# Kernel tuning notes

Measured on AMD Instinct MI355X. Metric: run time of the kernel, lower is better.

Reference implementation:

```python
import jax, jax.numpy as jnp
import numpy as np

N_NODES = 100000
N_EDGES = 1600000
F_IN, HIDDEN, N_CLS = 128, 128, 40


def _gcn_layer(h, W, b, src, dst, norm, n):
    # h: [n, d_in] -> linear transform then edge-normalized scatter-add
    h = h @ W                                   # [n, d_out]
    msg = h[src] * norm[:, None]                # gather over edges [E', d_out]
    out = jax.ops.segment_sum(msg, dst, num_segments=n)
    return out + b


def setup_inputs() -> dict:
    key = jax.random.key(0)
    k1, k2, k3, k4 = jax.random.split(key, 4)
    x = jax.random.normal(k1, (N_NODES, F_IN), dtype=jnp.float32)
    edge_index = jax.random.randint(k2, (2, N_EDGES), 0, N_NODES, dtype=jnp.int32)
    # glorot-style init
    W1 = jax.random.normal(k3, (F_IN, HIDDEN), dtype=jnp.float32) * (1.0 / np.sqrt(F_IN))
    W2 = jax.random.normal(k4, (HIDDEN, N_CLS), dtype=jnp.float32) * (1.0 / np.sqrt(HIDDEN))
    b1 = jnp.zeros((HIDDEN,), dtype=jnp.float32)
    b2 = jnp.zeros((N_CLS,), dtype=jnp.float32)
    return {"x": x, "edge_index": edge_index, "W1": W1, "b1": b1,
            "W2": W2, "b2": b2, "dropout": 0}


def reference(x, edge_index, W1, b1, W2, b2, dropout):
    n = x.shape[0]
    src, dst = edge_index[0], edge_index[1]
    # add self loops (PyG GCNConv default)
    loop = jnp.arange(n, dtype=src.dtype)
    src = jnp.concatenate([src, loop])
    dst = jnp.concatenate([dst, loop])
    # symmetric normalization D^{-1/2} (A+I) D^{-1/2}
    deg = jax.ops.segment_sum(jnp.ones(src.shape, dtype=x.dtype), dst, num_segments=n)
    dinv = jnp.where(deg > 0, jax.lax.rsqrt(deg), 0.0)
    norm = dinv[src] * dinv[dst]                # [E + n]
    h = jax.nn.relu(_gcn_layer(x, W1, b1, src, dst, norm, n))
    # F.dropout with training=False is identity (eval mode)
    return _gcn_layer(h, W2, b2, src, dst, norm, n)
```

## Files before the change

kernel.cpp:

```cpp
#include <hip/hip_runtime.h>
#include <stdint.h>


#define NF 128
#define NC 40
#define PSHIFT 7
#define PNODES 128
#define GH 256

typedef __attribute__((ext_vector_type(8))) short short8;
typedef __attribute__((ext_vector_type(4))) float float4m;

__device__ __forceinline__ float bflo2f(unsigned int u) {
  union { unsigned int i; float f; } v; v.i = u << 16; return v.f;
}
__device__ __forceinline__ float bfhi2f(unsigned int u) {
  union { unsigned int i; float f; } v; v.i = u & 0xffff0000u; return v.f;
}
__device__ __forceinline__ unsigned short f2bf(float f) {
  union { float f; unsigned int i; } v; v.f = f;
  unsigned int x = v.i;
  return (unsigned short)((x + 0x7fffu + ((x >> 16) & 1u)) >> 16);
}

__global__ __launch_bounds__(256) void hist_pack_k(
    const int* __restrict__ ei, int* __restrict__ histT, int E, int CPB, int NPART,
    const float* __restrict__ W1, const float* __restrict__ W2,
    unsigned short* __restrict__ Bpack, unsigned short* __restrict__ W2pack) {
  int tid = threadIdx.x, bid = blockIdx.x;
  if (bid >= GH) {
    int g = (bid - GH) * 256 + tid;
    const float* W; unsigned short* dst; int cols, frag;
    if (g < 2048)      { W = W1; dst = Bpack;  cols = 128; frag = g; }
    else if (g < 2816) { W = W2; dst = W2pack; cols = 40;  frag = g - 2048; }
    else return;
    int ct = frag >> 8, ks = (frag >> 6) & 3, lane = frag & 63;
    int quad = lane >> 4, l15 = lane & 15;
    int col = ct * 16 + l15, krow = ks * 32 + quad * 8;
    ushort4 lo = {0,0,0,0}, hi = {0,0,0,0};
    if (col < cols) {
      lo.x = f2bf(W[(krow + 0) * cols + col]);
      lo.y = f2bf(W[(krow + 1) * cols + col]);
      lo.z = f2bf(W[(krow + 2) * cols + col]);
      lo.w = f2bf(W[(krow + 3) * cols + col]);
      hi.x = f2bf(W[(krow + 4) * cols + col]);
      hi.y = f2bf(W[(krow + 5) * cols + col]);
      hi.z = f2bf(W[(krow + 6) * cols + col]);
      hi.w = f2bf(W[(krow + 7) * cols + col]);
    }
    *(ushort4*)&dst[(size_t)frag * 8 + 0] = lo;
    *(ushort4*)&dst[(size_t)frag * 8 + 4] = hi;
    return;
  }
  __shared__ int h[1024];
  for (int i = tid; i < NPART; i += 256) h[i] = 0;
  __syncthreads();
  int e0 = bid * CPB, e1 = min(e0 + CPB, E);
  for (int e = e0 + tid; e < e1; e += 256)
    atomicAdd(&h[ei[E + e] >> PSHIFT], 1);
  __syncthreads();
  for (int i = tid; i < NPART; i += 256) histT[(size_t)i * GH + bid] = h[i];
}

__global__ __launch_bounds__(256) void scanA_k(int* __restrict__ histT,
                                               int* __restrict__ partTotal) {
  __shared__ int sm[GH];
  int tid = threadIdx.x, p = blockIdx.x;
  int v = histT[(size_t)p * GH + tid];
  sm[tid] = v; __syncthreads();
  for (int off = 1; off < GH; off <<= 1) {
    int t = (tid >= off) ? sm[tid - off] : 0;
    __syncthreads();
    sm[tid] += t;
    __syncthreads();
  }
  histT[(size_t)p * GH + tid] = sm[tid] - v;
  if (tid == GH - 1) partTotal[p] = sm[GH - 1];
}

__global__ __launch_bounds__(1024) void scanB_k(const int* __restrict__ partTotal,
                                                int* __restrict__ base, int NPART) {
  __shared__ int sm[1024];
  int tid = threadIdx.x;
  int v = (tid < NPART) ? partTotal[tid] : 0;
  sm[tid] = v; __syncthreads();
  for (int off = 1; off < 1024; off <<= 1) {
    int t = (tid >= off) ? sm[tid - off] : 0;
    __syncthreads();
    sm[tid] += t;
    __syncthreads();
  }
  if (tid < NPART) base[tid] = sm[tid] - v;
}

__global__ __launch_bounds__(256) void scatter_k(const int* __restrict__ ei,
                                                 const int* __restrict__ histT,
                                                 const int* __restrict__ base,
                                                 unsigned int* __restrict__ epart,
                                                 int E, int CPB, int NPART) {
  __shared__ int off[1024];
  int tid = threadIdx.x, bid = blockIdx.x;
  for (int i = tid; i < NPART; i += 256)
    off[i] = base[i] + histT[(size_t)i * GH + bid];
  __syncthreads();
  int e0 = bid * CPB, e1 = min(e0 + CPB, E);
  for (int e = e0 + tid; e < e1; e += 256) {
    int s = ei[e], d = ei[E + e];
    int pos = atomicAdd(&off[d >> PSHIFT], 1);
    epart[pos] = ((unsigned int)(d & (PNODES - 1)) << 25) | (unsigned int)s;
  }
}

__global__ __launch_bounds__(256) void build_gemm_k(
    const float* __restrict__ x, const unsigned short* __restrict__ Bpack,
    unsigned short* __restrict__ Hs, const unsigned int* __restrict__ epart,
    const int* __restrict__ base, const int* __restrict__ partTotal,
    int* __restrict__ cnt, float* __restrict__ dinv,
    int* __restrict__ bucket, int n, int NPART, int G1) {
  __shared__ alignas(16) char smem[50176];
  int tid = threadIdx.x, bid = blockIdx.x;

  if (bid % 3 == 2) {
    int pidx = bid / 3;
    if (pidx >= NPART) return;
    int* lcnt = (int*)smem;
    int* lbuck = lcnt + PNODES;
    if (tid < PNODES) lcnt[tid] = 0;
    __syncthreads();
    int st = base[pidx], m = partTotal[pidx];
    for (int e = tid; e < m; e += 256) {
      unsigned int u = epart[(size_t)st + e];
      int ln = (int)(u >> 25), s = (int)(u & 0x1ffffffu);
      int pos = atomicAdd(&lcnt[ln], 1);
      if (pos < 64) lbuck[ln * 64 + pos] = s;
    }
    __syncthreads();
    int node0 = pidx << PSHIFT;
    int nn = min(PNODES, n - node0);
    int4* bg = (int4*)&bucket[(size_t)node0 * 64];
    const int4* bl = (const int4*)lbuck;
    for (int i = tid; i < nn * 16; i += 256) {
      int nd = i >> 4, q = i & 15;
      if (q * 4 < lcnt[nd]) bg[i] = bl[i];
    }
    if (tid < nn) {
      int c = lcnt[tid];
      cnt[node0 + tid] = c;
      dinv[node0 + tid] = rsqrtf((float)c + 1.0f);
    }
    return;
  }

  int idx = (bid / 3) * 2 + (bid % 3);
  if (idx >= G1) return;
  unsigned short* As = (unsigned short*)smem;
  unsigned short* Bs = (unsigned short*)(smem + 17408);
  int r0 = idx * 64;

  const float4* x4 = (const float4*)x;
  for (int i = tid; i < 2048; i += 256) {
    int kc = i & 31, r = i >> 5;
    float4 v = make_float4(0.f, 0.f, 0.f, 0.f);
    if (r0 + r < n) v = x4[(size_t)(r0 + r) * 32 + kc];
    ushort4 o;
    o.x = f2bf(v.x); o.y = f2bf(v.y); o.z = f2bf(v.z); o.w = f2bf(v.w);
    *(ushort4*)&As[r * 136 + kc * 4] = o;
  }
  {
    const uint4* bp4 = (const uint4*)Bpack;
    uint4* bs4 = (uint4*)Bs;
    for (int i = tid; i < 2048; i += 256) bs4[i] = bp4[i];
  }
  __syncthreads();

  int wv = tid >> 6, lane = tid & 63;
  int quad = lane >> 4, l15 = lane & 15;

  short8 afr[4];
#pragma unroll
  for (int ks = 0; ks < 4; ks++)
    afr[ks] = *(const short8*)&As[(wv * 16 + l15) * 136 + ks * 32 + quad * 8];

  float4m acc[8];
#pragma unroll
  for (int i = 0; i < 8; i++) acc[i] = (float4m){0.f, 0.f, 0.f, 0.f};

#pragma unroll
  for (int ct = 0; ct < 8; ct++) {
#pragma unroll
    for (int ks = 0; ks < 4; ks++) {
      short8 bfr = *(const short8*)&Bs[(((ct * 4 + ks) * 64) + lane) * 8];
      acc[ct] = __builtin_amdgcn_mfma_f32_16x16x32_bf16(afr[ks], bfr, acc[ct], 0, 0, 0);
    }
  }

  int rbase = r0 + wv * 16 + quad * 4;
#pragma unroll
  for (int ct = 0; ct < 8; ct++) {
#pragma unroll
    for (int reg = 0; reg < 4; reg++) {
      int r = rbase + reg;
      if (r < n) Hs[(size_t)r * 128 + ct * 16 + l15] = f2bf(acc[ct][reg]);
    }
  }
}

__global__ __launch_bounds__(256, 8) void agg1f_k(const unsigned int* __restrict__ Hs2,
                                               const int* __restrict__ cnt,
                                               const int* __restrict__ bucket,
                                               const float* __restrict__ dinv,
                                               const float2* __restrict__ b1v,
                                               const unsigned short* __restrict__ W2pack,
                                               unsigned short* __restrict__ H2s, int n) {
  __shared__ unsigned short As[16 * 136];
  __shared__ unsigned short W2s[768 * 8];
  int tid = threadIdx.x, wv = tid >> 6, lane = tid & 63;
  int node0 = blockIdx.x * 16;

  {
    const uint4* p = (const uint4*)W2pack;
    uint4* q = (uint4*)W2s;
    for (int i = tid; i < 768; i += 256) q[i] = p[i];
  }

  for (int s = 0; s < 4; s++) {
    int mrow = wv * 4 + s;
    int node = node0 + mrow;
    float r0 = 0.f, r1 = 0.f;
    if (node < n) {
      float d = dinv[node];
      unsigned int v = Hs2[(size_t)node * 64 + lane];
      float a0 = d * bflo2f(v), a1 = d * bfhi2f(v);
      int m = cnt[node]; if (m > 64) m = 64;
      const int* bp = &bucket[(size_t)node * 64];
      int p = 0;
      for (; p + 11 < m; p += 12) {
        int j0 = bp[p],   j1 = bp[p+1],  j2 = bp[p+2],  j3 = bp[p+3];
        int j4 = bp[p+4], j5 = bp[p+5],  j6 = bp[p+6],  j7 = bp[p+7];
        int j8 = bp[p+8], j9 = bp[p+9], j10 = bp[p+10], j11 = bp[p+11];
        float d0 = dinv[j0], d1 = dinv[j1], d2 = dinv[j2], d3 = dinv[j3];
        float d4 = dinv[j4], d5 = dinv[j5], d6 = dinv[j6], d7 = dinv[j7];
        float d8 = dinv[j8], d9 = dinv[j9], d10 = dinv[j10], d11 = dinv[j11];
        unsigned int u0 = Hs2[(size_t)j0 * 64 + lane];
        unsigned int u1 = Hs2[(size_t)j1 * 64 + lane];
        unsigned int u2 = Hs2[(size_t)j2 * 64 + lane];
        unsigned int u3 = Hs2[(size_t)j3 * 64 + lane];
        unsigned int u4 = Hs2[(size_t)j4 * 64 + lane];
        unsigned int u5 = Hs2[(size_t)j5 * 64 + lane];
        unsigned int u6 = Hs2[(size_t)j6 * 64 + lane];
        unsigned int u7 = Hs2[(size_t)j7 * 64 + lane];
        unsigned int u8 = Hs2[(size_t)j8 * 64 + lane];
        unsigned int u9 = Hs2[(size_t)j9 * 64 + lane];
        unsigned int u10 = Hs2[(size_t)j10 * 64 + lane];
        unsigned int u11 = Hs2[(size_t)j11 * 64 + lane];
        a0 += d0 * bflo2f(u0) + d1 * bflo2f(u1) + d2 * bflo2f(u2) + d3 * bflo2f(u3)
            + d4 * bflo2f(u4) + d5 * bflo2f(u5) + d6 * bflo2f(u6) + d7 * bflo2f(u7)
            + d8 * bflo2f(u8) + d9 * bflo2f(u9) + d10 * bflo2f(u10) + d11 * bflo2f(u11);
        a1 += d0 * bfhi2f(u0) + d1 * bfhi2f(u1) + d2 * bfhi2f(u2) + d3 * bfhi2f(u3)
            + d4 * bfhi2f(u4) + d5 * bfhi2f(u5) + d6 * bfhi2f(u6) + d7 * bfhi2f(u7)
            + d8 * bfhi2f(u8) + d9 * bfhi2f(u9) + d10 * bfhi2f(u10) + d11 * bfhi2f(u11);
      }
      for (; p + 3 < m; p += 4) {
        int j0 = bp[p], j1 = bp[p+1], j2 = bp[p+2], j3 = bp[p+3];
        float d0 = dinv[j0], d1 = dinv[j1], d2 = dinv[j2], d3 = dinv[j3];
        unsigned int u0 = Hs2[(size_t)j0 * 64 + lane];
        unsigned int u1 = Hs2[(size_t)j1 * 64 + lane];
        unsigned int u2 = Hs2[(size_t)j2 * 64 + lane];
        unsigned int u3 = Hs2[(size_t)j3 * 64 + lane];
        a0 += d0 * bflo2f(u0) + d1 * bflo2f(u1) + d2 * bflo2f(u2) + d3 * bflo2f(u3);
        a1 += d0 * bfhi2f(u0) + d1 * bfhi2f(u1) + d2 * bfhi2f(u2) + d3 * bfhi2f(u3);
      }
      for (; p < m; p++) {
        int j = bp[p];
        float dj = dinv[j];
        unsigned int u = Hs2[(size_t)j * 64 + lane];
        a0 += dj * bflo2f(u); a1 += dj * bfhi2f(u);
      }
      float2 bv = b1v[lane];
      r0 = fmaxf(0.0f, bv.x + d * a0);
      r1 = fmaxf(0.0f, bv.y + d * a1);
    }
    unsigned int pk = (unsigned int)f2bf(r0) | ((unsigned int)f2bf(r1) << 16);
    *(unsigned int*)&As[mrow * 136 + lane * 2] = pk;
  }
  __syncthreads();

  if (wv < 3) {
    int quad = lane >> 4, l15 = lane & 15;
    float4m acc = (float4m){0.f, 0.f, 0.f, 0.f};
#pragma unroll
    for (int ks = 0; ks < 4; ks++) {
      short8 afr = *(const short8*)&As[l15 * 136 + ks * 32 + quad * 8];
      short8 bfr = *(const short8*)&W2s[(((wv * 4 + ks) * 64) + lane) * 8];
      acc = __builtin_amdgcn_mfma_f32_16x16x32_bf16(afr, bfr, acc, 0, 0, 0);
    }
    int c = wv * 16 + l15;
    if (c < NC) {
#pragma unroll
      for (int reg = 0; reg < 4; reg++) {
        int node = node0 + quad * 4 + reg;
        if (node < n) {
          float dd = dinv[node];
          H2s[(size_t)node * 40 + c] = f2bf(acc[reg] * dd);
        }
      }
    }
  }
}

__global__ __launch_bounds__(256) void agg2_k(const unsigned int* __restrict__ H2u,
                                              const int* __restrict__ cnt,
                                              const int* __restrict__ bucket,
                                              const float* __restrict__ dinv,
                                              const float* __restrict__ b2,
                                              float* __restrict__ outp, int n) {
  int w = (blockIdx.x * 256 + threadIdx.x) >> 6;
  int lane = threadIdx.x & 63;
  int sub = lane / 20, ci = lane - sub * 20;
  int node = w * 3 + sub;
  if (sub >= 3 || node >= n) return;

  float d = dinv[node];
  unsigned int u = H2u[(size_t)node * 20 + ci];
  float a0 = bflo2f(u), a1 = bfhi2f(u);

  int m = cnt[node]; if (m > 64) m = 64;
  const int* bp = &bucket[(size_t)node * 64];
  int p = 0;
  for (; p + 7 < m; p += 8) {
    int j0 = bp[p],   j1 = bp[p+1], j2 = bp[p+2], j3 = bp[p+3];
    int j4 = bp[p+4], j5 = bp[p+5], j6 = bp[p+6], j7 = bp[p+7];
    unsigned int u0 = H2u[(size_t)j0*20+ci], u1 = H2u[(size_t)j1*20+ci];
    unsigned int u2 = H2u[(size_t)j2*20+ci], u3 = H2u[(size_t)j3*20+ci];
    unsigned int u4 = H2u[(size_t)j4*20+ci], u5 = H2u[(size_t)j5*20+ci];
    unsigned int u6 = H2u[(size_t)j6*20+ci], u7 = H2u[(size_t)j7*20+ci];
    a0 += bflo2f(u0)+bflo2f(u1)+bflo2f(u2)+bflo2f(u3)
        + bflo2f(u4)+bflo2f(u5)+bflo2f(u6)+bflo2f(u7);
    a1 += bfhi2f(u0)+bfhi2f(u1)+bfhi2f(u2)+bfhi2f(u3)
        + bfhi2f(u4)+bfhi2f(u5)+bfhi2f(u6)+bfhi2f(u7);
  }
  for (; p + 3 < m; p += 4) {
    int j0 = bp[p], j1 = bp[p+1], j2 = bp[p+2], j3 = bp[p+3];
    unsigned int u0 = H2u[(size_t)j0*20+ci], u1 = H2u[(size_t)j1*20+ci];
    unsigned int u2 = H2u[(size_t)j2*20+ci], u3 = H2u[(size_t)j3*20+ci];
    a0 += bflo2f(u0)+bflo2f(u1)+bflo2f(u2)+bflo2f(u3);
    a1 += bfhi2f(u0)+bfhi2f(u1)+bfhi2f(u2)+bfhi2f(u3);
  }
  for (; p < m; p++) {
    unsigned int uu = H2u[(size_t)bp[p]*20+ci];
    a0 += bflo2f(uu); a1 += bfhi2f(uu);
  }

  float2 o;
  o.x = b2[2 * ci]     + d * a0;
  o.y = b2[2 * ci + 1] + d * a1;
  *(float2*)&outp[(size_t)node * 40 + 2 * ci] = o;
}

extern "C" void kernel_launch(void* const* d_in, const int* in_sizes, int n_in,
                              void* d_out, int out_size, void* d_ws, size_t ws_size,
                              hipStream_t stream) {
  const float* x  = (const float*)d_in[0];
  const int*   ei = (const int*)d_in[1];
  const float* W1 = (const float*)d_in[2];
  const float* b1 = (const float*)d_in[3];
  const float* W2 = (const float*)d_in[4];
  const float* b2 = (const float*)d_in[5];

  int N = in_sizes[0] / NF;
  int E = in_sizes[1] / 2;
  int NPART = (N + PNODES - 1) >> PSHIFT;
  int CPB = (E + GH - 1) / GH;
  int G1 = (N + 63) / 64;

  char* ws = (char*)d_ws;
  size_t off = 0;
  auto carve = [&](size_t bytes) {
    void* p = ws + off;
    off += (bytes + 255) & ~(size_t)255;
    return p;
  };
  int*            cnt       = (int*)carve((size_t)N * 4);
  float*          dinv      = (float*)carve((size_t)N * 4);
  int*            bucket    = (int*)carve((size_t)N * 64 * 4);
  unsigned short* Hs        = (unsigned short*)carve((size_t)N * NF * 2);
  int*            histT     = (int*)carve((size_t)NPART * GH * 4);
  int*            partTotal = (int*)carve((size_t)NPART * 4);
  int*            base      = (int*)carve((size_t)NPART * 4);
  unsigned int*   epart     = (unsigned int*)carve((size_t)E * 4);
  unsigned short* Bpack     = (unsigned short*)carve(2048 * 8 * 2);
  unsigned short* W2pack    = (unsigned short*)carve(768 * 8 * 2);
  unsigned short* H2s       = (unsigned short*)carve((size_t)N * NC * 2);

  hist_pack_k<<<GH + 11, 256, 0, stream>>>(ei, histT, E, CPB, NPART,
                                           W1, W2, Bpack, W2pack);
  scanA_k<<<NPART, 256, 0, stream>>>(histT, partTotal);
  scanB_k<<<1, 1024, 0, stream>>>(partTotal, base, NPART);
  scatter_k<<<GH, 256, 0, stream>>>(ei, histT, base, epart, E, CPB, NPART);
  build_gemm_k<<<3 * NPART, 256, 0, stream>>>(x, Bpack, Hs, epart, base, partTotal,
                                              cnt, dinv, bucket, N, NPART, G1);
  agg1f_k<<<(N + 15) / 16, 256, 0, stream>>>((const unsigned int*)Hs, cnt, bucket,
                                             dinv, (const float2*)b1, W2pack, H2s, N);
  int NW = (N + 2) / 3;
  agg2_k<<<((size_t)NW * 64 + 255) / 256, 256, 0, stream>>>((const unsigned int*)H2s,
                                                            cnt, bucket, dinv, b2,
                                                            (float*)d_out, N);
}
```

Before: 270.1 us.

## Prescale features by dinv before GEMM and pad neighbor buckets to eight

Node degrees are now counted with global atomics in the histogram kernel, and dinv is computed early in scanA. This lets layer 1 fold the source-side normalization into the GEMM input by scaling rows of x by dinv. The per-edge dinv gathers in agg1 disappear, and neighbor lists are padded to multiples of eight with a dummy zero row at index N, so the gather loops read int4 index chunks without scalar tails. The cost is an extra memset, 1.6M global atomics on deg, and wasted loads on padded slots.

```diff
diff --git a/kernel.cpp b/kernel.cpp
--- a/kernel.cpp
+++ b/kernel.cpp
@@ -26,13 +26,17 @@
 __global__ __launch_bounds__(256) void hist_pack_k(
     const int* __restrict__ ei, int* __restrict__ histT, int E, int CPB, int NPART,
     const float* __restrict__ W1, const float* __restrict__ W2,
-    unsigned short* __restrict__ Bpack, unsigned short* __restrict__ W2pack) {
+    unsigned short* __restrict__ Bpack, unsigned short* __restrict__ W2pack,
+    int* __restrict__ deg, unsigned int* __restrict__ Hsu,
+    unsigned int* __restrict__ H2u, int n) {
   int tid = threadIdx.x, bid = blockIdx.x;
   if (bid >= GH) {
     int g = (bid - GH) * 256 + tid;
     const float* W; unsigned short* dst; int cols, frag;
     if (g < 2048)      { W = W1; dst = Bpack;  cols = 128; frag = g; }
     else if (g < 2816) { W = W2; dst = W2pack; cols = 40;  frag = g - 2048; }
+    else if (g < 2880) { Hsu[(size_t)n * 64 + (g - 2816)] = 0u; return; }
+    else if (g < 2900) { H2u[(size_t)n * 20 + (g - 2880)] = 0u; return; }
     else return;
     int ct = frag >> 8, ks = (frag >> 6) & 3, lane = frag & 63;
     int quad = lane >> 4, l15 = lane & 15;
@@ -56,16 +60,24 @@
   for (int i = tid; i < NPART; i += 256) h[i] = 0;
   __syncthreads();
   int e0 = bid * CPB, e1 = min(e0 + CPB, E);
-  for (int e = e0 + tid; e < e1; e += 256)
-    atomicAdd(&h[ei[E + e] >> PSHIFT], 1);
+  for (int e = e0 + tid; e < e1; e += 256) {
+    int d = ei[E + e];
+    atomicAdd(&h[d >> PSHIFT], 1);
+    atomicAdd(&deg[d], 1);
+  }
   __syncthreads();
   for (int i = tid; i < NPART; i += 256) histT[(size_t)i * GH + bid] = h[i];
 }
 
 __global__ __launch_bounds__(256) void scanA_k(int* __restrict__ histT,
-                                               int* __restrict__ partTotal) {
+                                               int* __restrict__ partTotal,
+                                               const int* __restrict__ deg,
+                                               float* __restrict__ dinv, int n) {
   __shared__ int sm[GH];
   int tid = threadIdx.x, p = blockIdx.x;
+  int node = (p << PSHIFT) + tid;
+  if (tid < PNODES && node < n)
+    dinv[node] = rsqrtf((float)deg[node] + 1.0f);
   int v = histT[(size_t)p * GH + tid];
   sm[tid] = v; __syncthreads();
   for (int off = 1; off < GH; off <<= 1) {
@@ -115,7 +127,7 @@
     const float* __restrict__ x, const unsigned short* __restrict__ Bpack,
     unsigned short* __restrict__ Hs, const unsigned int* __restrict__ epart,
     const int* __restrict__ base, const int* __restrict__ partTotal,
-    int* __restrict__ cnt, float* __restrict__ dinv,
+    const float* __restrict__ dinv,
     int* __restrict__ bucket, int n, int NPART, int G1) {
   __shared__ alignas(16) char smem[50176];
   int tid = threadIdx.x, bid = blockIdx.x;
@@ -137,16 +149,19 @@
     __syncthreads();
     int node0 = pidx << PSHIFT;
     int nn = min(PNODES, n - node0);
+    for (int i = tid; i < nn; i += 256) {
+      int c = lcnt[i]; if (c > 64) c = 64;
+      int c8 = (c + 7) & ~7; if (c8 > 64) c8 = 64;
+      for (int p = c; p < c8; p++) lbuck[i * 64 + p] = n;
+    }
+    __syncthreads();
     int4* bg = (int4*)&bucket[(size_t)node0 * 64];
     const int4* bl = (const int4*)lbuck;
     for (int i = tid; i < nn * 16; i += 256) {
       int nd = i >> 4, q = i & 15;
-      if (q * 4 < lcnt[nd]) bg[i] = bl[i];
-    }
-    if (tid < nn) {
-      int c = lcnt[tid];
-      cnt[node0 + tid] = c;
-      dinv[node0 + tid] = rsqrtf((float)c + 1.0f);
+      int c = lcnt[nd]; if (c > 64) c = 64;
+      int c8 = (c + 7) & ~7; if (c8 > 64) c8 = 64;
+      if (q * 4 < c8) bg[i] = bl[i];
     }
     return;
   }
@@ -161,7 +176,11 @@
   for (int i = tid; i < 2048; i += 256) {
     int kc = i & 31, r = i >> 5;
     float4 v = make_float4(0.f, 0.f, 0.f, 0.f);
-    if (r0 + r < n) v = x4[(size_t)(r0 + r) * 32 + kc];
+    if (r0 + r < n) {
+      float dr = dinv[r0 + r];
+      v = x4[(size_t)(r0 + r) * 32 + kc];
+      v.x *= dr; v.y *= dr; v.z *= dr; v.w *= dr;
+    }
     ushort4 o;
     o.x = f2bf(v.x); o.y = f2bf(v.y); o.z = f2bf(v.z); o.w = f2bf(v.w);
     *(ushort4*)&As[r * 136 + kc * 4] = o;
@@ -206,7 +225,7 @@
 }
 
 __global__ __launch_bounds__(256, 8) void agg1f_k(const unsigned int* __restrict__ Hs2,
-                                               const int* __restrict__ cnt,
+                                               const int* __restrict__ deg,
                                                const int* __restrict__ bucket,
                                                const float* __restrict__ dinv,
                                                const float2* __restrict__ b1v,
@@ -229,52 +248,54 @@
     float r0 = 0.f, r1 = 0.f;
     if (node < n) {
       float d = dinv[node];
-      unsigned int v = Hs2[(size_t)node * 64 + lane];
-      float a0 = d * bflo2f(v), a1 = d * bfhi2f(v);
-      int m = cnt[node]; if (m > 64) m = 64;
-      const int* bp = &bucket[(size_t)node * 64];
+      unsigned int v = Hs2[((unsigned)node << 6) + lane];
+      float a0 = bflo2f(v), a1 = bfhi2f(v);
+      int m = deg[node]; if (m > 64) m = 64;
+      int m8 = (m + 7) & ~7;
+      const int4* bq = (const int4*)&bucket[(size_t)node * 64];
       int p = 0;
-      for (; p + 11 < m; p += 12) {
-        int j0 = bp[p],   j1 = bp[p+1],  j2 = bp[p+2],  j3 = bp[p+3];
-        int j4 = bp[p+4], j5 = bp[p+5],  j6 = bp[p+6],  j7 = bp[p+7];
-        int j8 = bp[p+8], j9 = bp[p+9], j10 = bp[p+10], j11 = bp[p+11];
-        float d0 = dinv[j0], d1 = dinv[j1], d2 = dinv[j2], d3 = dinv[j3];
-        float d4 = dinv[j4], d5 = dinv[j5], d6 = dinv[j6], d7 = dinv[j7];
-        float d8 = dinv[j8], d9 = dinv[j9], d10 = dinv[j10], d11 = dinv[j11];
-        unsigned int u0 = Hs2[(size_t)j0 * 64 + lane];
-        unsigned int u1 = Hs2[(size_t)j1 * 64 + lane];
-        unsigned int u2 = Hs2[(size_t)j2 * 64 + lane];
-        unsigned int u3 = Hs2[(size_t)j3 * 64 + lane];
-        unsigned int u4 = Hs2[(size_t)j4 * 64 + lane];
-        unsigned int u5 = Hs2[(size_t)j5 * 64 + lane];
-        unsigned int u6 = Hs2[(size_t)j6 * 64 + lane];
-        unsigned int u7 = Hs2[(size_t)j7 * 64 + lane];
-        unsigned int u8 = Hs2[(size_t)j8 * 64 + lane];
-        unsigned int u9 = Hs2[(size_t)j9 * 64 + lane];
-        unsigned int u10 = Hs2[(size_t)j10 * 64 + lane];
-        unsigned int u11 = Hs2[(size_t)j11 * 64 + lane];
-        a0 += d0 * bflo2f(u0) + d1 * bflo2f(u1) + d2 * bflo2f(u2) + d3 * bflo2f(u3)
-            + d4 * bflo2f(u4) + d5 * bflo2f(u5) + d6 * bflo2f(u6) + d7 * bflo2f(u7)
-            + d8 * bflo2f(u8) + d9 * bflo2f(u9) + d10 * bflo2f(u10) + d11 * bflo2f(u11);
-        a1 += d0 * bfhi2f(u0) + d1 * bfhi2f(u1) + d2 * bfhi2f(u2) + d3 * bfhi2f(u3)
-            + d4 * bfhi2f(u4) + d5 * bfhi2f(u5) + d6 * bfhi2f(u6) + d7 * bfhi2f(u7)
-            + d8 * bfhi2f(u8) + d9 * bfhi2f(u9) + d10 * bfhi2f(u10) + d11 * bfhi2f(u11);
+      for (; p + 15 < m8; p += 16) {
+        int4 qa = bq[(p >> 2) + 0], qb = bq[(p >> 2) + 1];
+        int4 qc = bq[(p >> 2) + 2], qd = bq[(p >> 2) + 3];
+        unsigned int u0  = Hs2[((unsigned)qa.x << 6) + lane];
+        unsigned int u1  = Hs2[((unsigned)qa.y << 6) + lane];
+        unsigned int u2  = Hs2[((unsigned)qa.z << 6) + lane];
+        unsigned int u3  = Hs2[((unsigned)qa.w << 6) + lane];
+        unsigned int u4  = Hs2[((unsigned)qb.x << 6) + lane];
+        unsigned int u5  = Hs2[((unsigned)qb.y << 6) + lane];
+        unsigned int u6  = Hs2[((unsigned)qb.z << 6) + lane];
+        unsigned int u7  = Hs2[((unsigned)qb.w << 6) + lane];
+        unsigned int u8  = Hs2[((unsigned)qc.x << 6) + lane];
+        unsigned int u9  = Hs2[((unsigned)qc.y << 6) + lane];
+        unsigned int u10 = Hs2[((unsigned)qc.z << 6) + lane];
+        unsigned int u11 = Hs2[((unsigned)qc.w << 6) + lane];
+        unsigned int u12 = Hs2[((unsigned)qd.x << 6) + lane];
+        unsigned int u13 = Hs2[((unsigned)qd.y << 6) + lane];
+        unsigned int u14 = Hs2[((unsigned)qd.z << 6) + lane];
+        unsigned int u15 = Hs2[((unsigned)qd.w << 6) + lane];
+        a0 += bflo2f(u0)  + bflo2f(u1)  + bflo2f(u2)  + bflo2f(u3)
+            + bflo2f(u4)  + bflo2f(u5)  + bflo2f(u6)  + bflo2f(u7)
+            + bflo2f(u8)  + bflo2f(u9)  + bflo2f(u10) + bflo2f(u11)
+            + bflo2f(u12) + bflo2f(u13) + bflo2f(u14) + bflo2f(u15);
+        a1 += bfhi2f(u0)  + bfhi2f(u1)  + bfhi2f(u2)  + bfhi2f(u3)
+            + bfhi2f(u4)  + bfhi2f(u5)  + bfhi2f(u6)  + bfhi2f(u7)
+            + bfhi2f(u8)  + bfhi2f(u9)  + bfhi2f(u10) + bfhi2f(u11)
+            + bfhi2f(u12) + bfhi2f(u13) + bfhi2f(u14) + bfhi2f(u15);
       }
-      for (; p + 3 < m; p += 4) {
-        int j0 = bp[p], j1 = bp[p+1], j2 = bp[p+2], j3 = bp[p+3];
-        float d0 = dinv[j0], d1 = dinv[j1], d2 = dinv[j2], d3 = dinv[j3];
-        unsigned int u0 = Hs2[(size_t)j0 * 64 + lane];
-        unsigned int u1 = Hs2[(size_t)j1 * 64 + lane];
-        unsigned int u2 = Hs2[(size_t)j2 * 64 + lane];
-        unsigned int u3 = Hs2[(size_t)j3 * 64 + lane];
-        a0 += d0 * bflo2f(u0) + d1 * bflo2f(u1) + d2 * bflo2f(u2) + d3 * bflo2f(u3);
-        a1 += d0 * bfhi2f(u0) + d1 * bfhi2f(u1) + d2 * bfhi2f(u2) + d3 * bfhi2f(u3);
-      }
-      for (; p < m; p++) {
-        int j = bp[p];
-        float dj = dinv[j];
-        unsigned int u = Hs2[(size_t)j * 64 + lane];
-        a0 += dj * bflo2f(u); a1 += dj * bfhi2f(u);
+      if (p < m8) {
+        int4 qa = bq[(p >> 2) + 0], qb = bq[(p >> 2) + 1];
+        unsigned int u0 = Hs2[((unsigned)qa.x << 6) + lane];
+        unsigned int u1 = Hs2[((unsigned)qa.y << 6) + lane];
+        unsigned int u2 = Hs2[((unsigned)qa.z << 6) + lane];
+        unsigned int u3 = Hs2[((unsigned)qa.w << 6) + lane];
+        unsigned int u4 = Hs2[((unsigned)qb.x << 6) + lane];
+        unsigned int u5 = Hs2[((unsigned)qb.y << 6) + lane];
+        unsigned int u6 = Hs2[((unsigned)qb.z << 6) + lane];
+        unsigned int u7 = Hs2[((unsigned)qb.w << 6) + lane];
+        a0 += bflo2f(u0) + bflo2f(u1) + bflo2f(u2) + bflo2f(u3)
+            + bflo2f(u4) + bflo2f(u5) + bflo2f(u6) + bflo2f(u7);
+        a1 += bfhi2f(u0) + bfhi2f(u1) + bfhi2f(u2) + bfhi2f(u3)
+            + bfhi2f(u4) + bfhi2f(u5) + bfhi2f(u6) + bfhi2f(u7);
       }
       float2 bv = b1v[lane];
       r0 = fmaxf(0.0f, bv.x + d * a0);
@@ -309,7 +330,7 @@
 }
 
 __global__ __launch_bounds__(256) void agg2_k(const unsigned int* __restrict__ H2u,
-                                              const int* __restrict__ cnt,
+                                              const int* __restrict__ deg,
                                               const int* __restrict__ bucket,
                                               const float* __restrict__ dinv,
                                               const float* __restrict__ b2,
@@ -321,34 +342,26 @@
   if (sub >= 3 || node >= n) return;
 
   float d = dinv[node];
-  unsigned int u = H2u[(size_t)node * 20 + ci];
+  unsigned int u = H2u[(unsigned)node * 20 + ci];
   float a0 = bflo2f(u), a1 = bfhi2f(u);
 
-  int m = cnt[node]; if (m > 64) m = 64;
-  const int* bp = &bucket[(size_t)node * 64];
-  int p = 0;
-  for (; p + 7 < m; p += 8) {
-    int j0 = bp[p],   j1 = bp[p+1], j2 = bp[p+2], j3 = bp[p+3];
-    int j4 = bp[p+4], j5 = bp[p+5], j6 = bp[p+6], j7 = bp[p+7];
-    unsigned int u0 = H2u[(size_t)j0*20+ci], u1 = H2u[(size_t)j1*20+ci];
-    unsigned int u2 = H2u[(size_t)j2*20+ci], u3 = H2u[(size_t)j3*20+ci];
-    unsigned int u4 = H2u[(size_t)j4*20+ci], u5 = H2u[(size_t)j5*20+ci];
-    unsigned int u6 = H2u[(size_t)j6*20+ci], u7 = H2u[(size_t)j7*20+ci];
+  int m = deg[node]; if (m > 64) m = 64;
+  int m8 = (m + 7) & ~7;
+  const int4* bq = (const int4*)&bucket[(size_t)node * 64];
+  for (int p = 0; p < m8; p += 8) {
+    int4 qa = bq[(p >> 2) + 0], qb = bq[(p >> 2) + 1];
+    unsigned int u0 = H2u[(unsigned)qa.x * 20 + ci];
+    unsigned int u1 = H2u[(unsigned)qa.y * 20 + ci];
+    unsigned int u2 = H2u[(unsigned)qa.z * 20 + ci];
+    unsigned int u3 = H2u[(unsigned)qa.w * 20 + ci];
+    unsigned int u4 = H2u[(unsigned)qb.x * 20 + ci];
+    unsigned int u5 = H2u[(unsigned)qb.y * 20 + ci];
+    unsigned int u6 = H2u[(unsigned)qb.z * 20 + ci];
+    unsigned int u7 = H2u[(unsigned)qb.w * 20 + ci];
     a0 += bflo2f(u0)+bflo2f(u1)+bflo2f(u2)+bflo2f(u3)
         + bflo2f(u4)+bflo2f(u5)+bflo2f(u6)+bflo2f(u7);
     a1 += bfhi2f(u0)+bfhi2f(u1)+bfhi2f(u2)+bfhi2f(u3)
         + bfhi2f(u4)+bfhi2f(u5)+bfhi2f(u6)+bfhi2f(u7);
-  }
-  for (; p + 3 < m; p += 4) {
-    int j0 = bp[p], j1 = bp[p+1], j2 = bp[p+2], j3 = bp[p+3];
-    unsigned int u0 = H2u[(size_t)j0*20+ci], u1 = H2u[(size_t)j1*20+ci];
-    unsigned int u2 = H2u[(size_t)j2*20+ci], u3 = H2u[(size_t)j3*20+ci];
-    a0 += bflo2f(u0)+bflo2f(u1)+bflo2f(u2)+bflo2f(u3);
-    a1 += bfhi2f(u0)+bfhi2f(u1)+bfhi2f(u2)+bfhi2f(u3);
-  }
-  for (; p < m; p++) {
-    unsigned int uu = H2u[(size_t)bp[p]*20+ci];
-    a0 += bflo2f(uu); a1 += bfhi2f(uu);
   }
 
   float2 o;
@@ -380,29 +393,32 @@
     off += (bytes + 255) & ~(size_t)255;
     return p;
   };
-  int*            cnt       = (int*)carve((size_t)N * 4);
+  int*            deg       = (int*)carve((size_t)N * 4);
   float*          dinv      = (float*)carve((size_t)N * 4);
   int*            bucket    = (int*)carve((size_t)N * 64 * 4);
-  unsigned short* Hs        = (unsigned short*)carve((size_t)N * NF * 2);
+  unsigned short* Hs        = (unsigned short*)carve((size_t)(N + 1) * NF * 2);
   int*            histT     = (int*)carve((size_t)NPART * GH * 4);
   int*            partTotal = (int*)carve((size_t)NPART * 4);
   int*            base      = (int*)carve((size_t)NPART * 4);
   unsigned int*   epart     = (unsigned int*)carve((size_t)E * 4);
   unsigned short* Bpack     = (unsigned short*)carve(2048 * 8 * 2);
   unsigned short* W2pack    = (unsigned short*)carve(768 * 8 * 2);
-  unsigned short* H2s       = (unsigned short*)carve((size_t)N * NC * 2);
-
-  hist_pack_k<<<GH + 11, 256, 0, stream>>>(ei, histT, E, CPB, NPART,
-                                           W1, W2, Bpack, W2pack);
-  scanA_k<<<NPART, 256, 0, stream>>>(histT, partTotal);
+  unsigned short* H2s       = (unsigned short*)carve((size_t)(N + 1) * NC * 2);
+
+  hipMemsetAsync(deg, 0, (size_t)N * 4, stream);
+  hist_pack_k<<<GH + 12, 256, 0, stream>>>(ei, histT, E, CPB, NPART,
+                                           W1, W2, Bpack, W2pack,
+                                           deg, (unsigned int*)Hs,
+                                           (unsigned int*)H2s, N);
+  scanA_k<<<NPART, 256, 0, stream>>>(histT, partTotal, deg, dinv, N);
   scanB_k<<<1, 1024, 0, stream>>>(partTotal, base, NPART);
   scatter_k<<<GH, 256, 0, stream>>>(ei, histT, base, epart, E, CPB, NPART);
   build_gemm_k<<<3 * NPART, 256, 0, stream>>>(x, Bpack, Hs, epart, base, partTotal,
-                                              cnt, dinv, bucket, N, NPART, G1);
-  agg1f_k<<<(N + 15) / 16, 256, 0, stream>>>((const unsigned int*)Hs, cnt, bucket,
+                                              dinv, bucket, N, NPART, G1);
+  agg1f_k<<<(N + 15) / 16, 256, 0, stream>>>((const unsigned int*)Hs, deg, bucket,
                                              dinv, (const float2*)b1, W2pack, H2s, N);
   int NW = (N + 2) / 3;
   agg2_k<<<((size_t)NW * 64 + 255) / 256, 256, 0, stream>>>((const unsigned int*)H2s,
-                                                            cnt, bucket, dinv, b2,
+                                                            deg, bucket, dinv, b2,
                                                             (float*)d_out, N);
 }
```

Result: slower. 311.9 us (+15.4%).
